# Kernel optimization log

Hardware: AMD Instinct MI355X
Metric: run time of the kernel (lower is better)

Reference implementation:

```python
import jax, jax.numpy as jnp
import numpy as np
from jax.ops import segment_sum, segment_max

N_NODES = 50000
N_EDGES = 800000
D_IN = 128
HEADS = 4
D_HEAD = 32
OUT_DIM = 512
NEG_SLOPE = 0.2
EPS = 1e-9


def setup_inputs() -> dict:
    key = jax.random.key(0)
    ks = jax.random.split(key, 12)
    h = jax.random.normal(ks[0], (N_NODES, D_IN), dtype=jnp.float32)
    src = jax.random.randint(ks[1], (N_EDGES,), 0, N_NODES, dtype=jnp.int32)
    dst = jax.random.randint(ks[2], (N_EDGES,), 0, N_NODES, dtype=jnp.int32)
    s = 0.1
    W1 = jax.random.normal(ks[3], (D_IN, HEADS * D_HEAD), dtype=jnp.float32) * s
    al1 = jax.random.normal(ks[4], (HEADS, D_HEAD), dtype=jnp.float32) * s
    ar1 = jax.random.normal(ks[5], (HEADS, D_HEAD), dtype=jnp.float32) * s
    b1 = jnp.zeros((HEADS * D_HEAD,), dtype=jnp.float32)
    W2 = jax.random.normal(ks[6], (HEADS * D_HEAD, HEADS * D_HEAD), dtype=jnp.float32) * s
    al2 = jax.random.normal(ks[7], (HEADS, D_HEAD), dtype=jnp.float32) * s
    ar2 = jax.random.normal(ks[8], (HEADS, D_HEAD), dtype=jnp.float32) * s
    b2 = jnp.zeros((HEADS * D_HEAD,), dtype=jnp.float32)
    Wp = jax.random.normal(ks[9], (D_HEAD, OUT_DIM), dtype=jnp.float32) * s
    bp = jnp.zeros((OUT_DIM,), dtype=jnp.float32)
    return {"h": h, "src": src, "dst": dst, "W1": W1, "al1": al1, "ar1": ar1,
            "b1": b1, "W2": W2, "al2": al2, "ar2": ar2, "b2": b2,
            "Wp": Wp, "bp": bp}


def gat_layer(h, W, a_l, a_r, b, src, dst, agg):
    # h: [N, Din]; W: [Din, H*Dh]; a_l/a_r: [H, Dh]; b: [H*Dh]
    N = h.shape[0]
    Wh = (h @ W).reshape(N, HEADS, D_HEAD)            # [N, H, Dh]
    el = jnp.einsum('nhd,hd->nh', Wh, a_l)            # [N, H]
    er = jnp.einsum('nhd,hd->nh', Wh, a_r)            # [N, H]
    e = el[src] + er[dst]                             # [E, H]
    e = jnp.where(e > 0, e, NEG_SLOPE * e)            # LeakyReLU(0.2)
    m = segment_max(e, dst, num_segments=N)           # [N, H]
    m = jnp.where(jnp.isfinite(m), m, 0.0)            # empty segments
    ex = jnp.exp(e - m[dst])                          # [E, H]
    denom = segment_sum(ex, dst, num_segments=N)      # [N, H]
    alpha = ex / (denom[dst] + EPS)                   # [E, H]
    msg = alpha[:, :, None] * Wh[src]                 # [E, H, Dh]
    out = segment_sum(msg, dst, num_segments=N)       # [N, H, Dh]
    out = out + b.reshape(HEADS, D_HEAD)
    if agg == 'flatten':
        return out.reshape(N, HEADS * D_HEAD)
    return out.mean(axis=1)                           # 'mean' for last layer


def reference(h, src, dst, W1, al1, ar1, b1, W2, al2, ar2, b2, Wp, bp):
    src = src.astype(jnp.int32)
    dst = dst.astype(jnp.int32)
    z = gat_layer(h, W1, al1, ar1, b1, src, dst, agg='flatten')
    z = jax.nn.elu(z)
    z = gat_layer(z, W2, al2, ar2, b2, src, dst, agg='mean')  # [N, Dh]
    return z @ Wp + bp                                        # [N, OUT_DIM]
```

## Files before the change

### kernel.cpp

```cpp
#include <hip/hip_runtime.h>
#include <hip/hip_bf16.h>
#include <math.h>

#define HEADS 4
#define D_HEAD 32
#define HD 128
#define D_IN 128
#define OUT_DIM 512
#define NEG_SLOPE 0.2f
#define EPS 1e-9f
#define LOG2E 1.4426950408889634f
#define MAXD 64

typedef float f32x4 __attribute__((ext_vector_type(4)));
typedef float f32x2 __attribute__((ext_vector_type(2)));
typedef short bf16x8 __attribute__((ext_vector_type(8)));
typedef unsigned short u16x8 __attribute__((ext_vector_type(8)));

#if defined(__has_builtin)
#if __has_builtin(__builtin_amdgcn_exp2f)
#define EXP2(x) __builtin_amdgcn_exp2f(x)
#else
#define EXP2(x) exp2f(x)
#endif
#else
#define EXP2(x) exp2f(x)
#endif

__device__ __forceinline__ float lrelu(float x) { return x > 0.f ? x : NEG_SLOPE * x; }

__device__ __forceinline__ unsigned short f2bf(float f)
{
    union { float f; unsigned int u; } v; v.f = f;
    unsigned int r = (v.u + 0x7FFFu + ((v.u >> 16) & 1u)) >> 16;
    return (unsigned short)r;
}
__device__ __forceinline__ float bf2f(unsigned short b)
{
    union { unsigned int u; float f; } v; v.u = ((unsigned int)b) << 16;
    return v.f;
}

__global__ void setup(const float* __restrict__ W1, const float* __restrict__ W2,
                      unsigned short* __restrict__ Wt1, unsigned short* __restrict__ Wt2,
                      int* __restrict__ cnt, int N)
{
    int idx = blockIdx.x * 256 + threadIdx.x;
    if (idx < 16384) {
        int k = idx >> 7, c = idx & 127;
        Wt1[(size_t)c * 128 + k] = f2bf(W1[idx]);
    } else if (idx < 32768) {
        int i = idx - 16384;
        int k = i >> 7, c = i & 127;
        Wt2[(size_t)c * 128 + k] = f2bf(W2[i]);
    } else {
        int i = idx - 32768;
        if (i < N) cnt[i] = 0;
    }
}

__global__ void scatter_padded(const int* __restrict__ src, const int* __restrict__ dst,
                               int* __restrict__ cnt, int* __restrict__ colp, int E)
{
    int e = blockIdx.x * 256 + threadIdx.x;
    if (e >= E) return;
    int d = dst[e];
    int p = atomicAdd(&cnt[d], 1);
    if (p < MAXD) colp[(size_t)d * MAXD + p] = src[e];
}

template <int BF16IN>
__global__ __launch_bounds__(256) void gemm_mfma(
    const void* __restrict__ Xv, const unsigned short* __restrict__ Wt,
    const float* __restrict__ al, const float* __restrict__ ar,
    unsigned short* __restrict__ Wh, float* __restrict__ el, float* __restrict__ er, int N)
{
    __shared__ unsigned short Xs[32 * 128];
    __shared__ unsigned short Wts[128 * 128];

    const int tid = threadIdx.x;
    const int node0 = blockIdx.x * 32;

    {
        const uint4* src = (const uint4*)Wt;
#pragma unroll
        for (int i = 0; i < 8; ++i) {
            int f = tid + 256 * i;
            int row = f >> 4;
            int byte = (f << 4) ^ ((row & 7) << 4);
            *(uint4*)((char*)Wts + byte) = src[f];
        }
    }
    {
#pragma unroll
        for (int i = 0; i < 2; ++i) {
            int f = tid + 256 * i;
            int row = f >> 4, kc = f & 15;
            int n = node0 + row;
            int byte = (f << 4) ^ ((row & 7) << 4);
            if (BF16IN) {
                uint4 v = make_uint4(0, 0, 0, 0);
                if (n < N)
                    v = *(const uint4*)((const unsigned short*)Xv + (size_t)n * 128 + kc * 8);
                *(uint4*)((char*)Xs + byte) = v;
            } else {
                u16x8 v = {0, 0, 0, 0, 0, 0, 0, 0};
                if (n < N) {
                    const float* xp = (const float*)Xv + (size_t)n * 128 + kc * 8;
                    float4 f0 = *(const float4*)xp;
                    float4 f1 = *(const float4*)(xp + 4);
                    v[0] = f2bf(f0.x); v[1] = f2bf(f0.y); v[2] = f2bf(f0.z); v[3] = f2bf(f0.w);
                    v[4] = f2bf(f1.x); v[5] = f2bf(f1.y); v[6] = f2bf(f1.z); v[7] = f2bf(f1.w);
                }
                *(u16x8*)((char*)Xs + byte) = v;
            }
        }
    }
    __syncthreads();

    const int w  = tid >> 6;
    const int l  = tid & 63;
    const int lr = l & 15;
    const int lg = l >> 4;

    f32x4 zero4 = {0.f, 0.f, 0.f, 0.f};
    f32x4 acc[2][2];
    acc[0][0] = zero4; acc[0][1] = zero4; acc[1][0] = zero4; acc[1][1] = zero4;

    const int c0 = w * 32 + lr, c1 = w * 32 + 16 + lr;
    const int rA0 = lr, rA1 = 16 + lr;

#pragma unroll
    for (int ks = 0; ks < 4; ++ks) {
        const int kb2 = ks * 64 + lg * 16;
        bf16x8 a0 = *(const bf16x8*)((char*)Xs  + ((rA0 * 256 + kb2) ^ ((rA0 & 7) << 4)));
        bf16x8 a1 = *(const bf16x8*)((char*)Xs  + ((rA1 * 256 + kb2) ^ ((rA1 & 7) << 4)));
        bf16x8 b0 = *(const bf16x8*)((char*)Wts + ((c0  * 256 + kb2) ^ ((c0  & 7) << 4)));
        bf16x8 b1 = *(const bf16x8*)((char*)Wts + ((c1  * 256 + kb2) ^ ((c1  & 7) << 4)));
        acc[0][0] = __builtin_amdgcn_mfma_f32_16x16x32_bf16(a0, b0, acc[0][0], 0, 0, 0);
        acc[0][1] = __builtin_amdgcn_mfma_f32_16x16x32_bf16(a0, b1, acc[0][1], 0, 0, 0);
        acc[1][0] = __builtin_amdgcn_mfma_f32_16x16x32_bf16(a1, b0, acc[1][0], 0, 0, 0);
        acc[1][1] = __builtin_amdgcn_mfma_f32_16x16x32_bf16(a1, b1, acc[1][1], 0, 0, 0);
    }

    const float alv0 = al[w * 32 + lr], alv1 = al[w * 32 + 16 + lr];
    const float arv0 = ar[w * 32 + lr], arv1 = ar[w * 32 + 16 + lr];

#pragma unroll
    for (int rt = 0; rt < 2; ++rt) {
#pragma unroll
        for (int r = 0; r < 4; ++r) {
            const int n = node0 + rt * 16 + lg * 4 + r;
            if (n < N) {
                Wh[(size_t)n * 128 + w * 32 + lr]      = f2bf(acc[rt][0][r]);
                Wh[(size_t)n * 128 + w * 32 + 16 + lr] = f2bf(acc[rt][1][r]);
            }
            float pl = acc[rt][0][r] * alv0 + acc[rt][1][r] * alv1;
            float pr = acc[rt][0][r] * arv0 + acc[rt][1][r] * arv1;
#pragma unroll
            for (int off = 1; off < 16; off <<= 1) {
                pl += __shfl_xor(pl, off, 16);
                pr += __shfl_xor(pr, off, 16);
            }
            if (lr == 0 && n < N) {
                el[(size_t)n * 4 + w] = pl;
                er[(size_t)n * 4 + w] = pr;
            }
        }
    }
}

template <int MODE>
__global__ __launch_bounds__(256) void gat_node(
    const int* __restrict__ cnt, const int* __restrict__ colp,
    const float* __restrict__ el, const float* __restrict__ er,
    const unsigned short* __restrict__ Wh, const float* __restrict__ bias,
    void* __restrict__ out, int N)
{
    const int wave = threadIdx.x >> 6;
    const int lane = threadIdx.x & 63;
    const int n = blockIdx.x * 4 + wave;
    if (n >= N) return;

    const int deg   = min(cnt[n], MAXD);
    const int start = n * MAXD;
    const int end   = start + deg;

    const int sub = lane >> 5;
    const int q   = lane & 31;
    const int h2  = q >> 3;
    const float erv = er[(size_t)n * 4 + h2];

    float4 acc0 = make_float4(0.f, 0.f, 0.f, 0.f);
    float4 acc1 = make_float4(0.f, 0.f, 0.f, 0.f);
    float4 acc2 = make_float4(0.f, 0.f, 0.f, 0.f);
    float4 acc3 = make_float4(0.f, 0.f, 0.f, 0.f);
    float d0 = 0.f, d1 = 0.f, d2 = 0.f, d3 = 0.f;

#define GAT_EDGE(JJ, ACC, DEN) do {                                            \
        int s_ = colp[(JJ)];                                                   \
        float e_ = lrelu(el[(size_t)s_ * 4 + h2] + erv);                       \
        float p_ = EXP2(e_ * LOG2E);                                           \
        ushort4 w_ = *(const ushort4*)(Wh + (size_t)s_ * 128 + 4 * q);         \
        ACC.x += p_ * bf2f(w_.x); ACC.y += p_ * bf2f(w_.y);                    \
        ACC.z += p_ * bf2f(w_.z); ACC.w += p_ * bf2f(w_.w);                    \
        DEN += p_;                                                             \
    } while (0)

    int j = start + sub;
    for (; j + 6 < end; j += 8) {
        GAT_EDGE(j,     acc0, d0);
        GAT_EDGE(j + 2, acc1, d1);
        GAT_EDGE(j + 4, acc2, d2);
        GAT_EDGE(j + 6, acc3, d3);
    }
    for (; j < end; j += 2)
        GAT_EDGE(j, acc0, d0);
#undef GAT_EDGE

    float4 acc;
    acc.x = (acc0.x + acc1.x) + (acc2.x + acc3.x);
    acc.y = (acc0.y + acc1.y) + (acc2.y + acc3.y);
    acc.z = (acc0.z + acc1.z) + (acc2.z + acc3.z);
    acc.w = (acc0.w + acc1.w) + (acc2.w + acc3.w);
    float denom = (d0 + d1) + (d2 + d3);

    acc.x += __shfl_xor(acc.x, 32, 64);
    acc.y += __shfl_xor(acc.y, 32, 64);
    acc.z += __shfl_xor(acc.z, 32, 64);
    acc.w += __shfl_xor(acc.w, 32, 64);
    denom += __shfl_xor(denom, 32, 64);

    const float inv = 1.f / (denom + EPS);
    acc.x *= inv; acc.y *= inv; acc.z *= inv; acc.w *= inv;

    const float4 bv = *(const float4*)(bias + 4 * q);
    if (MODE == 0) {
        if (sub == 0) {
            float x;
            ushort4 ob;
            x = acc.x + bv.x; ob.x = f2bf(x > 0.f ? x : expm1f(x));
            x = acc.y + bv.y; ob.y = f2bf(x > 0.f ? x : expm1f(x));
            x = acc.z + bv.z; ob.z = f2bf(x > 0.f ? x : expm1f(x));
            x = acc.w + bv.w; ob.w = f2bf(x > 0.f ? x : expm1f(x));
            *(ushort4*)((unsigned short*)out + (size_t)n * 128 + 4 * q) = ob;
        }
    } else {
        float x = acc.x + bv.x, y = acc.y + bv.y, z = acc.z + bv.z, w = acc.w + bv.w;
        x += __shfl_xor(x, 8, 64);  x += __shfl_xor(x, 16, 64);
        y += __shfl_xor(y, 8, 64);  y += __shfl_xor(y, 16, 64);
        z += __shfl_xor(z, 8, 64);  z += __shfl_xor(z, 16, 64);
        w += __shfl_xor(w, 8, 64);  w += __shfl_xor(w, 16, 64);
        if (lane < 8) {
            float4 o = make_float4(0.25f * x, 0.25f * y, 0.25f * z, 0.25f * w);
            *(float4*)((float*)out + (size_t)n * 32 + 4 * q) = o;
        }
    }
}

#define PROJ_NB 2048
__device__ __forceinline__ void proj_load(const float* __restrict__ z2, int n, float4* z)
{
#pragma unroll
    for (int i = 0; i < 8; ++i)
        z[i] = *(const float4*)(z2 + (size_t)n * 32 + i * 4);
}

__device__ __forceinline__ f32x2 proj_comp(const float4* z, const float2* wp, float2 bv)
{
    float x = bv.x, y = bv.y;
#pragma unroll
    for (int k4 = 0; k4 < 8; ++k4) {
        float4 zz = z[k4];
        x += zz.x * wp[4 * k4 + 0].x; y += zz.x * wp[4 * k4 + 0].y;
        x += zz.y * wp[4 * k4 + 1].x; y += zz.y * wp[4 * k4 + 1].y;
        x += zz.z * wp[4 * k4 + 2].x; y += zz.z * wp[4 * k4 + 2].y;
        x += zz.w * wp[4 * k4 + 3].x; y += zz.w * wp[4 * k4 + 3].y;
    }
    f32x2 o; o.x = x; o.y = y;
    return o;
}

__global__ __launch_bounds__(256) void proj(
    const float* __restrict__ z2, const float* __restrict__ Wp,
    const float* __restrict__ bp, float* __restrict__ out, int N)
{
    const int wave = threadIdx.x >> 6;
    const int lane = threadIdx.x & 63;
    const int c0 = wave * 128 + lane * 2;

    const int per = (N + PROJ_NB - 1) / PROJ_NB;
    int n  = blockIdx.x * per;
    const int nE = min(n + per, N);
    if (n >= nE) return;

    float2 wp[32];
#pragma unroll
    for (int k = 0; k < 32; ++k)
        wp[k] = *(const float2*)(Wp + (size_t)k * 512 + c0);
    const float2 bv = *(const float2*)(bp + c0);

    float4 zA[8], zB[8];
    proj_load(z2, n, zA);

    for (; n + 2 <= nE; n += 2) {
        proj_load(z2, n + 1, zB);
        f32x2 oA = proj_comp(zA, wp, bv);
        __builtin_nontemporal_store(oA, (f32x2*)(out + (size_t)n * 512 + c0));
        if (n + 2 < nE) proj_load(z2, n + 2, zA);
        f32x2 oB = proj_comp(zB, wp, bv);
        __builtin_nontemporal_store(oB, (f32x2*)(out + (size_t)(n + 1) * 512 + c0));
    }
    if (n < nE) {
        f32x2 oA = proj_comp(zA, wp, bv);
        __builtin_nontemporal_store(oA, (f32x2*)(out + (size_t)n * 512 + c0));
    }
}

extern "C" void kernel_launch(void* const* d_in, const int* in_sizes, int n_in,
                              void* d_out, int out_size, void* d_ws, size_t ws_size,
                              hipStream_t stream)
{
    const float* h   = (const float*)d_in[0];
    const int*   src = (const int*)d_in[1];
    const int*   dst = (const int*)d_in[2];
    const float* W1  = (const float*)d_in[3];
    const float* al1 = (const float*)d_in[4];
    const float* ar1 = (const float*)d_in[5];
    const float* b1  = (const float*)d_in[6];
    const float* W2  = (const float*)d_in[7];
    const float* al2 = (const float*)d_in[8];
    const float* ar2 = (const float*)d_in[9];
    const float* b2  = (const float*)d_in[10];
    const float* Wp  = (const float*)d_in[11];
    const float* bp  = (const float*)d_in[12];
    float* out = (float*)d_out;

    const int N = in_sizes[0] / D_IN;
    const int E = in_sizes[1];

    float* ws = (float*)d_ws;
    size_t off = 0;
    unsigned short* Wh = (unsigned short*)(ws + off); off += (size_t)N * 64;
    unsigned short* z  = (unsigned short*)(ws + off); off += (size_t)N * 64;
    float* z2   = ws + off; off += (size_t)N * 32;
    float* el   = ws + off; off += (size_t)N * 4;
    float* er   = ws + off; off += (size_t)N * 4;
    int* cnt    = (int*)(ws + off); off += (size_t)N;
    int* colp   = (int*)(ws + off); off += (size_t)N * MAXD;
    unsigned short* Wt1 = (unsigned short*)(ws + off); off += 8192;
    unsigned short* Wt2 = (unsigned short*)(ws + off); off += 8192;

    const int gemm_grid = (N + 31) / 32;
    const int edge_grid = (E + 255) / 256;
    const int node_grid = (N + 3) / 4;

    setup<<<(32768 + N + 255) / 256, 256, 0, stream>>>(W1, W2, Wt1, Wt2, cnt, N);
    scatter_padded<<<edge_grid, 256, 0, stream>>>(src, dst, cnt, colp, E);

    gemm_mfma<0><<<gemm_grid, 256, 0, stream>>>(h, Wt1, al1, ar1, Wh, el, er, N);
    gat_node<0><<<node_grid, 256, 0, stream>>>(cnt, colp, el, er, Wh, b1, z, N);

    gemm_mfma<1><<<gemm_grid, 256, 0, stream>>>(z, Wt2, al2, ar2, Wh, el, er, N);
    gat_node<1><<<node_grid, 256, 0, stream>>>(cnt, colp, el, er, Wh, b2, z2, N);

    proj<<<PROJ_NB, 256, 0, stream>>>(z2, Wp, bp, out, N);
}
```

Baseline: 313.1 us.

## Merge edge scatter into first GEMM launch and widen per-lane gather vectors

The first projection GEMM and the edge bucketing scatter now share one launch, with block ranges split between them so the two independent tasks run concurrently and one launch is removed. The scatter handles four edges per thread using int4 loads. The node aggregation kernel now has each lane load 8 bf16 features (16 bytes) instead of 4, and processes four edges at a time per wave with 16 lanes per row, reducing the number of iterations. In exchange, the reductions need more shuffles, each lane keeps more live registers, and the fused kernel reserves the GEMM's shared memory even for scatter blocks.

```diff
diff --git a/kernel.cpp b/kernel.cpp
--- a/kernel.cpp
+++ b/kernel.cpp
@@ -59,28 +59,13 @@
     }
 }
 
-__global__ void scatter_padded(const int* __restrict__ src, const int* __restrict__ dst,
-                               int* __restrict__ cnt, int* __restrict__ colp, int E)
-{
-    int e = blockIdx.x * 256 + threadIdx.x;
-    if (e >= E) return;
-    int d = dst[e];
-    int p = atomicAdd(&cnt[d], 1);
-    if (p < MAXD) colp[(size_t)d * MAXD + p] = src[e];
-}
-
 template <int BF16IN>
-__global__ __launch_bounds__(256) void gemm_mfma(
+__device__ __forceinline__ void gemm_core(
+    unsigned short* Xs, unsigned short* Wts, int tid, int node0,
     const void* __restrict__ Xv, const unsigned short* __restrict__ Wt,
     const float* __restrict__ al, const float* __restrict__ ar,
     unsigned short* __restrict__ Wh, float* __restrict__ el, float* __restrict__ er, int N)
 {
-    __shared__ unsigned short Xs[32 * 128];
-    __shared__ unsigned short Wts[128 * 128];
-
-    const int tid = threadIdx.x;
-    const int node0 = blockIdx.x * 32;
-
     {
         const uint4* src = (const uint4*)Wt;
 #pragma unroll
@@ -170,6 +155,50 @@
     }
 }
 
+__global__ __launch_bounds__(256) void gemm1_scatter(
+    const float* __restrict__ h, const unsigned short* __restrict__ Wt1,
+    const float* __restrict__ al, const float* __restrict__ ar,
+    unsigned short* __restrict__ Wh, float* __restrict__ el, float* __restrict__ er, int N,
+    const int* __restrict__ src, const int* __restrict__ dst,
+    int* __restrict__ cnt, int* __restrict__ colp, int E, int GB)
+{
+    __shared__ unsigned short Xs[32 * 128];
+    __shared__ unsigned short Wts[128 * 128];
+
+    if (blockIdx.x < GB) {
+        gemm_core<0>(Xs, Wts, threadIdx.x, blockIdx.x * 32, h, Wt1, al, ar, Wh, el, er, N);
+        return;
+    }
+    int t = (blockIdx.x - GB) * 256 + threadIdx.x;
+    int base = t * 4;
+    if (base >= E) return;
+    if (base + 4 <= E) {
+        int4 s4 = ((const int4*)src)[t];
+        int4 d4 = ((const int4*)dst)[t];
+        int p;
+        p = atomicAdd(&cnt[d4.x], 1); if (p < MAXD) colp[(size_t)d4.x * MAXD + p] = s4.x;
+        p = atomicAdd(&cnt[d4.y], 1); if (p < MAXD) colp[(size_t)d4.y * MAXD + p] = s4.y;
+        p = atomicAdd(&cnt[d4.z], 1); if (p < MAXD) colp[(size_t)d4.z * MAXD + p] = s4.z;
+        p = atomicAdd(&cnt[d4.w], 1); if (p < MAXD) colp[(size_t)d4.w * MAXD + p] = s4.w;
+    } else {
+        for (int e = base; e < E; ++e) {
+            int d = dst[e];
+            int p = atomicAdd(&cnt[d], 1);
+            if (p < MAXD) colp[(size_t)d * MAXD + p] = src[e];
+        }
+    }
+}
+
+__global__ __launch_bounds__(256) void gemm_mfma2(
+    const unsigned short* __restrict__ z, const unsigned short* __restrict__ Wt2,
+    const float* __restrict__ al, const float* __restrict__ ar,
+    unsigned short* __restrict__ Wh, float* __restrict__ el, float* __restrict__ er, int N)
+{
+    __shared__ unsigned short Xs[32 * 128];
+    __shared__ unsigned short Wts[128 * 128];
+    gemm_core<1>(Xs, Wts, threadIdx.x, blockIdx.x * 32, z, Wt2, al, ar, Wh, el, er, N);
+}
+
 template <int MODE>
 __global__ __launch_bounds__(256) void gat_node(
     const int* __restrict__ cnt, const int* __restrict__ colp,
@@ -186,74 +215,78 @@
     const int start = n * MAXD;
     const int end   = start + deg;
 
-    const int sub = lane >> 5;
-    const int q   = lane & 31;
-    const int h2  = q >> 3;
+    const int g  = lane >> 4;
+    const int r  = lane & 15;
+    const int h2 = r >> 2;
     const float erv = er[(size_t)n * 4 + h2];
 
-    float4 acc0 = make_float4(0.f, 0.f, 0.f, 0.f);
-    float4 acc1 = make_float4(0.f, 0.f, 0.f, 0.f);
-    float4 acc2 = make_float4(0.f, 0.f, 0.f, 0.f);
-    float4 acc3 = make_float4(0.f, 0.f, 0.f, 0.f);
-    float d0 = 0.f, d1 = 0.f, d2 = 0.f, d3 = 0.f;
+    float accA[8] = {0.f, 0.f, 0.f, 0.f, 0.f, 0.f, 0.f, 0.f};
+    float accB[8] = {0.f, 0.f, 0.f, 0.f, 0.f, 0.f, 0.f, 0.f};
+    float dA = 0.f, dB = 0.f;
 
 #define GAT_EDGE(JJ, ACC, DEN) do {                                            \
         int s_ = colp[(JJ)];                                                   \
         float e_ = lrelu(el[(size_t)s_ * 4 + h2] + erv);                       \
         float p_ = EXP2(e_ * LOG2E);                                           \
-        ushort4 w_ = *(const ushort4*)(Wh + (size_t)s_ * 128 + 4 * q);         \
-        ACC.x += p_ * bf2f(w_.x); ACC.y += p_ * bf2f(w_.y);                    \
-        ACC.z += p_ * bf2f(w_.z); ACC.w += p_ * bf2f(w_.w);                    \
+        u16x8 w_ = *(const u16x8*)(Wh + (size_t)s_ * 128 + 8 * r);             \
+        ACC[0] += p_ * bf2f(w_[0]); ACC[1] += p_ * bf2f(w_[1]);                \
+        ACC[2] += p_ * bf2f(w_[2]); ACC[3] += p_ * bf2f(w_[3]);                \
+        ACC[4] += p_ * bf2f(w_[4]); ACC[5] += p_ * bf2f(w_[5]);                \
+        ACC[6] += p_ * bf2f(w_[6]); ACC[7] += p_ * bf2f(w_[7]);                \
         DEN += p_;                                                             \
     } while (0)
 
-    int j = start + sub;
-    for (; j + 6 < end; j += 8) {
-        GAT_EDGE(j,     acc0, d0);
-        GAT_EDGE(j + 2, acc1, d1);
-        GAT_EDGE(j + 4, acc2, d2);
-        GAT_EDGE(j + 6, acc3, d3);
-    }
-    for (; j < end; j += 2)
-        GAT_EDGE(j, acc0, d0);
+    int j = start + g;
+    for (; j + 4 < end; j += 8) {
+        GAT_EDGE(j, accA, dA);
+        GAT_EDGE(j + 4, accB, dB);
+    }
+    if (j < end) GAT_EDGE(j, accA, dA);
 #undef GAT_EDGE
 
-    float4 acc;
-    acc.x = (acc0.x + acc1.x) + (acc2.x + acc3.x);
-    acc.y = (acc0.y + acc1.y) + (acc2.y + acc3.y);
-    acc.z = (acc0.z + acc1.z) + (acc2.z + acc3.z);
-    acc.w = (acc0.w + acc1.w) + (acc2.w + acc3.w);
-    float denom = (d0 + d1) + (d2 + d3);
-
-    acc.x += __shfl_xor(acc.x, 32, 64);
-    acc.y += __shfl_xor(acc.y, 32, 64);
-    acc.z += __shfl_xor(acc.z, 32, 64);
-    acc.w += __shfl_xor(acc.w, 32, 64);
-    denom += __shfl_xor(denom, 32, 64);
-
-    const float inv = 1.f / (denom + EPS);
-    acc.x *= inv; acc.y *= inv; acc.z *= inv; acc.w *= inv;
-
-    const float4 bv = *(const float4*)(bias + 4 * q);
+    float acc[8];
+#pragma unroll
+    for (int i = 0; i < 8; ++i) acc[i] = accA[i] + accB[i];
+    float den = dA + dB;
+
+#pragma unroll
+    for (int i = 0; i < 8; ++i) {
+        acc[i] += __shfl_xor(acc[i], 16, 64);
+        acc[i] += __shfl_xor(acc[i], 32, 64);
+    }
+    den += __shfl_xor(den, 16, 64);
+    den += __shfl_xor(den, 32, 64);
+
+    const float inv = 1.f / (den + EPS);
+    const float4 bv0 = *(const float4*)(bias + 8 * r);
+    const float4 bv1 = *(const float4*)(bias + 8 * r + 4);
+    float x[8];
+    x[0] = acc[0] * inv + bv0.x; x[1] = acc[1] * inv + bv0.y;
+    x[2] = acc[2] * inv + bv0.z; x[3] = acc[3] * inv + bv0.w;
+    x[4] = acc[4] * inv + bv1.x; x[5] = acc[5] * inv + bv1.y;
+    x[6] = acc[6] * inv + bv1.z; x[7] = acc[7] * inv + bv1.w;
+
     if (MODE == 0) {
-        if (sub == 0) {
-            float x;
-            ushort4 ob;
-            x = acc.x + bv.x; ob.x = f2bf(x > 0.f ? x : expm1f(x));
-            x = acc.y + bv.y; ob.y = f2bf(x > 0.f ? x : expm1f(x));
-            x = acc.z + bv.z; ob.z = f2bf(x > 0.f ? x : expm1f(x));
-            x = acc.w + bv.w; ob.w = f2bf(x > 0.f ? x : expm1f(x));
-            *(ushort4*)((unsigned short*)out + (size_t)n * 128 + 4 * q) = ob;
+        if (g == 0) {
+            u16x8 ob;
+#pragma unroll
+            for (int i = 0; i < 8; ++i) {
+                float v = x[i] > 0.f ? x[i] : expm1f(x[i]);
+                ob[i] = f2bf(v);
+            }
+            *(u16x8*)((unsigned short*)out + (size_t)n * 128 + 8 * r) = ob;
         }
     } else {
-        float x = acc.x + bv.x, y = acc.y + bv.y, z = acc.z + bv.z, w = acc.w + bv.w;
-        x += __shfl_xor(x, 8, 64);  x += __shfl_xor(x, 16, 64);
-        y += __shfl_xor(y, 8, 64);  y += __shfl_xor(y, 16, 64);
-        z += __shfl_xor(z, 8, 64);  z += __shfl_xor(z, 16, 64);
-        w += __shfl_xor(w, 8, 64);  w += __shfl_xor(w, 16, 64);
-        if (lane < 8) {
-            float4 o = make_float4(0.25f * x, 0.25f * y, 0.25f * z, 0.25f * w);
-            *(float4*)((float*)out + (size_t)n * 32 + 4 * q) = o;
+#pragma unroll
+        for (int i = 0; i < 8; ++i) {
+            x[i] += __shfl_xor(x[i], 4, 64);
+            x[i] += __shfl_xor(x[i], 8, 64);
+        }
+        if (g == 0 && r < 4) {
+            float4 o0 = make_float4(0.25f * x[0], 0.25f * x[1], 0.25f * x[2], 0.25f * x[3]);
+            float4 o1 = make_float4(0.25f * x[4], 0.25f * x[5], 0.25f * x[6], 0.25f * x[7]);
+            *(float4*)((float*)out + (size_t)n * 32 + 8 * r)     = o0;
+            *(float4*)((float*)out + (size_t)n * 32 + 8 * r + 4) = o1;
         }
     }
 }
@@ -352,16 +385,17 @@
     unsigned short* Wt2 = (unsigned short*)(ws + off); off += 8192;
 
     const int gemm_grid = (N + 31) / 32;
-    const int edge_grid = (E + 255) / 256;
+    const int scat_grid = ((E + 3) / 4 + 255) / 256;
     const int node_grid = (N + 3) / 4;
 
     setup<<<(32768 + N + 255) / 256, 256, 0, stream>>>(W1, W2, Wt1, Wt2, cnt, N);
-    scatter_padded<<<edge_grid, 256, 0, stream>>>(src, dst, cnt, colp, E);
-
-    gemm_mfma<0><<<gemm_grid, 256, 0, stream>>>(h, Wt1, al1, ar1, Wh, el, er, N);
+
+    gemm1_scatter<<<gemm_grid + scat_grid, 256, 0, stream>>>(
+        h, Wt1, al1, ar1, Wh, el, er, N, src, dst, cnt, colp, E, gemm_grid);
+
     gat_node<0><<<node_grid, 256, 0, stream>>>(cnt, colp, el, er, Wh, b1, z, N);
 
-    gemm_mfma<1><<<gemm_grid, 256, 0, stream>>>(z, Wt2, al2, ar2, Wh, el, er, N);
+    gemm_mfma2<<<gemm_grid, 256, 0, stream>>>(z, Wt2, al2, ar2, Wh, el, er, N);
     gat_node<1><<<node_grid, 256, 0, stream>>>(cnt, colp, el, er, Wh, b2, z2, N);
 
     proj<<<PROJ_NB, 256, 0, stream>>>(z2, Wp, bp, out, N);
```

Result: faster. 306.5 us (-2.1%).
